# Kernel optimization log

Hardware: AMD Instinct MI355X
Metric: run time of the kernel (lower is better)

## Reference

```python
import jax, jax.numpy as jnp
import numpy as np

B, N, K, C = 2, 4096, 2048, 16
DSPAN, E, H, V = 2048, 300, 512, 100000
WEIGHT = 1.0


def setup_inputs() -> dict:
    key = jax.random.key(0)
    ks = jax.random.split(key, 10)
    return {
        "cand_span_vecs": jax.random.normal(ks[0], (B, N, DSPAN), jnp.float32),
        "targets_all": jax.random.uniform(ks[1], (B, N, C), jnp.float32),
        "entity_emb": jax.random.normal(ks[2], (V, E), jnp.float32) * 0.02,
        "W1": jax.random.normal(ks[3], (DSPAN + E, H), jnp.float32) * 0.02,
        "b1": jnp.zeros((H,), jnp.float32),
        "W2": jax.random.normal(ks[4], (H, 1), jnp.float32) * 0.02,
        "b2": jnp.zeros((1,), jnp.float32),
        "linker_indices_hoi": jax.random.randint(ks[5], (B, K), 0, N, jnp.int64),
        "candidates_all": jax.random.randint(ks[6], (B, N, C), 0, V, jnp.int64),
        "candidate_lengths_all": jax.random.randint(ks[7], (B, N), 0, C + 1, jnp.int64),
    }


def reference(cand_span_vecs, targets_all, entity_emb, W1, b1, W2, b2,
              linker_indices_hoi, candidates_all, candidate_lengths_all):
    idx = linker_indices_hoi  # [B, K]
    # batched_index_select over the span axis
    candidates = jnp.take_along_axis(candidates_all, idx[:, :, None], axis=1)      # [B,K,C]
    cand_lens = jnp.take_along_axis(candidate_lengths_all, idx, axis=1)            # [B,K]
    targets = jnp.take_along_axis(targets_all, idx[:, :, None], axis=1)            # [B,K,C]
    linker_vecs = jnp.take_along_axis(cand_span_vecs, idx[:, :, None], axis=1)     # [B,K,Dspan]
    # entity embedding lookup
    candidate_vecs = entity_emb[candidates]                                        # [B,K,C,E]
    # expand span vecs over candidate axis and concat
    span_exp = jnp.broadcast_to(linker_vecs[:, :, None, :],
                                (linker_vecs.shape[0], linker_vecs.shape[1],
                                 candidate_vecs.shape[2], linker_vecs.shape[2]))
    vecs = jnp.concatenate([span_exp, candidate_vecs], axis=-1)                    # [B,K,C,Dspan+E]
    # FFNN: Linear -> ReLU -> (dropout is identity in eval) -> Linear
    h = jax.nn.relu(jnp.einsum('bkcd,dh->bkch', vecs, W1) + b1)
    scores = (jnp.einsum('bkch,ho->bkco', h, W2) + b2)[..., 0]                     # [B,K,C]
    # candidate mask: valid where position < candidate_length
    mask = (jnp.arange(scores.shape[-1]) < cand_lens[:, :, None]).astype(scores.dtype)
    # BCEWithLogits (reduction='none'): softplus(x) - x*t
    bce = jax.nn.softplus(scores) - scores * targets
    obj = (mask * bce).sum() * WEIGHT
    return obj
```

## Files before the change

kernel.cpp:

```cpp
#include <hip/hip_runtime.h>
#include <math.h>

#define NN 4096
#define CC 16
#define DSP 2048
#define ED 300
#define HD 512

typedef __attribute__((ext_vector_type(8))) short short8;
typedef __attribute__((ext_vector_type(4))) float f32x4;

#define MFMA16(a, b, c) __builtin_amdgcn_mfma_f32_16x16x32_bf16((a), (b), (c), 0, 0, 0)

__device__ __forceinline__ unsigned short f2bf(float x) {
    unsigned u = __builtin_bit_cast(unsigned, x);
    u += 0x7FFFu + ((u >> 16) & 1u);
    return (unsigned short)(u >> 16);
}

__device__ __forceinline__ float bf2f(unsigned short u) {
    return __builtin_bit_cast(float, (unsigned)u << 16);
}

__device__ __forceinline__ void gl_lds16(const void* g, void* l) {
    __builtin_amdgcn_global_load_lds(
        (const __attribute__((address_space(1))) unsigned*)g,
        (__attribute__((address_space(3))) unsigned*)l, 16, 0, 0);
}

__device__ __forceinline__ void pack8(unsigned short* dst, float4 a, float4 b) {
    unsigned short v[8] = { f2bf(a.x), f2bf(a.y), f2bf(a.z), f2bf(a.w),
                            f2bf(b.x), f2bf(b.y), f2bf(b.z), f2bf(b.w) };
    *(short8*)dst = *(short8*)v;
}

__global__ __launch_bounds__(256) void prep_gather_scan(
    const float* __restrict__ W1,
    const float* __restrict__ span,
    const int*   __restrict__ lidx,
    const int*   __restrict__ clens,
    unsigned short* __restrict__ W1sT,
    unsigned short* __restrict__ w1ef,
    unsigned short* __restrict__ A16,
    int*            __restrict__ off)
{
    const int bid = blockIdx.x, tid = threadIdx.x;

    if (bid == 4432) {
        __shared__ int ls[256];
        int myl[16];
        int msum = 0;
#pragma unroll
        for (int j = 0; j < 16; ++j) {
            int bk = tid * 16 + j;
            size_t base = (size_t)(bk >> 11) * NN + lidx[bk];
            int len = clens[base];
            len = len < 0 ? 0 : (len > CC ? CC : len);
            myl[j] = len; msum += len;
        }
        ls[tid] = msum;
        __syncthreads();
        for (int d = 1; d < 256; d <<= 1) {
            int v = (tid >= d) ? ls[tid - d] : 0;
            __syncthreads();
            ls[tid] += v;
            __syncthreads();
        }
        int run = ls[tid] - msum;
#pragma unroll
        for (int j = 0; j < 16; ++j) { off[tid * 16 + j] = run; run += myl[j]; }
        if (tid == 255) off[4096] = run;
        return;
    }
    if (bid >= 336) {
        const int bk = bid - 336;
        const float* src = span + ((size_t)(bk >> 11) * NN + lidx[bk]) * DSP;
        float4 x = *(const float4*)(src + tid * 8);
        float4 y = *(const float4*)(src + tid * 8 + 4);
        pack8(&A16[(size_t)bk * DSP + tid * 8], x, y);
        return;
    }
    if (bid < 256) {
        __shared__ float t[64][65];
        const int k0 = (bid >> 3) * 64, n0 = (bid & 7) * 64;
#pragma unroll
        for (int p = 0; p < 16; ++p) {
            int flat = p * 256 + tid;
            int r = flat >> 6, c = flat & 63;
            t[r][c] = W1[(size_t)(k0 + r) * HD + n0 + c];
        }
        __syncthreads();
#pragma unroll
        for (int p = 0; p < 16; ++p) {
            int flat = p * 256 + tid;
            int c = flat >> 6, r = flat & 63;
            W1sT[(size_t)(n0 + c) * DSP + k0 + r] = f2bf(t[r][c]);
        }
    } else {
        int t0 = (bid - 256) * 256 + tid;
        int lane = t0 & 63;
        int ks = (t0 >> 6) % 10;
        int ncg = (t0 >> 6) / 10;
        int col = ncg * 16 + (lane & 15);
        int kb = ks * 32 + ((lane >> 4) << 3);
        unsigned short v[8];
#pragma unroll
        for (int j = 0; j < 8; ++j) {
            int k = kb + j;
            v[j] = (k < ED) ? f2bf(W1[(size_t)(DSP + k) * HD + col]) : (unsigned short)0;
        }
        *(short8*)&w1ef[(size_t)t0 * 8] = *(short8*)v;
    }
}

__global__ __launch_bounds__(256) void gemm_and_fill(
    const unsigned short* __restrict__ A16,
    const unsigned short* __restrict__ BT,
    const float* __restrict__ b1,
    unsigned short* __restrict__ Cout,
    const int* __restrict__ lidx,
    const int* __restrict__ cands,
    const int* __restrict__ clens,
    const int* __restrict__ off,
    int* __restrict__ compact_cand,
    int* __restrict__ compact_meta)
{
    const int tid = threadIdx.x;

    if (blockIdx.x >= 512) {
        int fb = blockIdx.x - 512;
        int item0 = (fb * 256 + tid) * 4;
#pragma unroll
        for (int q = 0; q < 4; ++q) {
            int item = item0 + q;
            int bk = item >> 4, c = item & 15;
            size_t base = (size_t)(bk >> 11) * NN + lidx[bk];
            int len = clens[base];
            len = len > CC ? CC : len;
            if (c < len) {
                int pos = off[bk] + c;
                compact_cand[pos] = cands[base * CC + c];
                compact_meta[pos] = item;
            }
        }
        return;
    }

    __shared__ __align__(16) unsigned short As[4][64 * 64];
    __shared__ __align__(16) unsigned short Bs[4][64 * 64];
    const int l = tid & 63, wid = tid >> 6;
    const int wr = (wid >> 1) * 32, wc = (wid & 1) * 32;

    const int bid = blockIdx.x;
    const int brow = ((bid & 7) * 8 + ((bid >> 3) >> 3)) * 64;
    const int bcol = (((bid >> 3) & 7)) * 64;

    const int s0 = tid, s1 = tid + 256;
    const int r0 = s0 >> 3, c0 = ((s0 & 7) ^ (r0 & 7)) * 8;
    const int r1 = s1 >> 3, c1 = ((s1 & 7) ^ (r1 & 7)) * 8;
    const unsigned short* ga0 = A16 + (size_t)(brow + r0) * DSP + c0;
    const unsigned short* ga1 = A16 + (size_t)(brow + r1) * DSP + c1;
    const unsigned short* gb0 = BT + (size_t)(bcol + r0) * DSP + c0;
    const unsigned short* gb1 = BT + (size_t)(bcol + r1) * DSP + c1;

    int offA[2][2], offB[2][2];
#pragma unroll
    for (int mf = 0; mf < 2; ++mf) {
        int row = wr + mf * 16 + (l & 15);
#pragma unroll
        for (int kk = 0; kk < 2; ++kk)
            offA[mf][kk] = row * 64 + (((kk * 4) + (l >> 4)) ^ (row & 7)) * 8;
    }
#pragma unroll
    for (int nf = 0; nf < 2; ++nf) {
        int row = wc + nf * 16 + (l & 15);
#pragma unroll
        for (int kk = 0; kk < 2; ++kk)
            offB[nf][kk] = row * 64 + (((kk * 4) + (l >> 4)) ^ (row & 7)) * 8;
    }

    f32x4 z = {0.f, 0.f, 0.f, 0.f};
    f32x4 acc[2][2] = {{z, z}, {z, z}};

    auto stage = [&](int buf, int t) {
        const int k0 = t * 64;
        gl_lds16(ga0 + k0, &As[buf][s0 * 8]);
        gl_lds16(ga1 + k0, &As[buf][s1 * 8]);
        gl_lds16(gb0 + k0, &Bs[buf][s0 * 8]);
        gl_lds16(gb1 + k0, &Bs[buf][s1 * 8]);
    };

    auto compute = [&](int buf) {
        short8 am[2][2], bn[2][2];
#pragma unroll
        for (int mf = 0; mf < 2; ++mf)
#pragma unroll
            for (int kk = 0; kk < 2; ++kk)
                am[mf][kk] = *(const short8*)&As[buf][offA[mf][kk]];
#pragma unroll
        for (int nf = 0; nf < 2; ++nf)
#pragma unroll
            for (int kk = 0; kk < 2; ++kk)
                bn[nf][kk] = *(const short8*)&Bs[buf][offB[nf][kk]];
#pragma unroll
        for (int m = 0; m < 2; ++m)
#pragma unroll
            for (int n = 0; n < 2; ++n)
#pragma unroll
                for (int kk = 0; kk < 2; ++kk)
                    acc[m][n] = MFMA16(am[m][kk], bn[n][kk], acc[m][n]);
    };

    stage(0, 0);
    stage(1, 1);
    stage(2, 2);

    for (int t = 0; t < 29; ++t) {
        asm volatile("s_waitcnt vmcnt(8)" ::: "memory");
        __builtin_amdgcn_s_barrier();
        stage((t + 3) & 3, t + 3);
        compute(t & 3);
    }
    asm volatile("s_waitcnt vmcnt(8)" ::: "memory");
    __builtin_amdgcn_s_barrier();
    compute(29 & 3);
    asm volatile("s_waitcnt vmcnt(4)" ::: "memory");
    __builtin_amdgcn_s_barrier();
    compute(30 & 3);
    asm volatile("s_waitcnt vmcnt(0)" ::: "memory");
    __builtin_amdgcn_s_barrier();
    compute(31 & 3);

#pragma unroll
    for (int n = 0; n < 2; ++n) {
        int col = bcol + wc + n * 16 + (l & 15);
        float b1v = b1[col];
#pragma unroll
        for (int m = 0; m < 2; ++m) {
            int row0 = brow + wr + m * 16 + (l >> 4) * 4;
#pragma unroll
            for (int r = 0; r < 4; ++r)
                Cout[(size_t)(row0 + r) * HD + col] = f2bf(acc[m][n][r] + b1v);
        }
    }
}

__global__ __launch_bounds__(512) void ent_mfma(
    const unsigned short* __restrict__ w1ef,
    const unsigned short* __restrict__ span_part,
    const float* __restrict__ emb,
    const float* __restrict__ W2,
    const float* __restrict__ b2,
    const int*   __restrict__ lidx,
    const float* __restrict__ targets,
    const int*   __restrict__ compact_cand,
    const int*   __restrict__ compact_meta,
    const int*   __restrict__ off,
    float* __restrict__ blockPartial)
{
    const int total = off[4096];
    const int bid = blockIdx.x;
    const int slotBase = bid * 128;
    const int tid = threadIdx.x;
    if (slotBase >= total) {
        if (tid == 0) blockPartial[bid] = 0.f;
        return;
    }

    __shared__ __align__(16) unsigned short As[2][8 * 64 * 8];
    __shared__ float shp[8][16][8];
    __shared__ int   meta_s[128];
    __shared__ float wred[8];
    const int wid = tid >> 6, l = tid & 63;

    if (tid < 128) {
        int slot = slotBase + tid;
        meta_s[tid] = (slot < total) ? compact_meta[slot] : -1;
    }

    const int slot_s = slotBase + wid * 16 + (l & 15);
    const int cid = (slot_s < total) ? compact_cand[slot_s] : 0;
    const float* erow = emb + (size_t)cid * ED;
    const int kb = (l >> 4) * 8;
    const int ht = wid;

    float4 lx = *(const float4*)(erow + kb);
    float4 ly = *(const float4*)(erow + kb + 4);
    pack8(&As[0][tid * 8], lx, ly);
    __syncthreads();

    f32x4 z = {0.f, 0.f, 0.f, 0.f};
    f32x4 acc[8][4];
#pragma unroll
    for (int g = 0; g < 8; ++g)
#pragma unroll
        for (int nc = 0; nc < 4; ++nc) acc[g][nc] = z;

    int cur = 0;
    for (int ks = 0; ks < 10; ++ks) {
        const bool pf = (ks < 9);
        if (pf) {
            int k = (ks + 1) * 32 + kb;
            if (k + 8 <= ED) {
                lx = *(const float4*)(erow + k);
                ly = *(const float4*)(erow + k + 4);
            } else {
                float tmp[8];
#pragma unroll
                for (int j = 0; j < 8; ++j) tmp[j] = (k + j < ED) ? erow[k + j] : 0.f;
                lx = make_float4(tmp[0], tmp[1], tmp[2], tmp[3]);
                ly = make_float4(tmp[4], tmp[5], tmp[6], tmp[7]);
            }
        }
        short8 af[8];
#pragma unroll
        for (int g = 0; g < 8; ++g)
            af[g] = *(const short8*)&As[cur][(g * 64 + l) * 8];
#pragma unroll
        for (int nc = 0; nc < 4; ++nc) {
            short8 bf = *(const short8*)&w1ef[(((size_t)(ht * 4 + nc) * 10 + ks) * 64 + l) * 8];
#pragma unroll
            for (int g = 0; g < 8; ++g)
                acc[g][nc] = MFMA16(af[g], bf, acc[g][nc]);
        }
        if (pf) {
            pack8(&As[cur ^ 1][tid * 8], lx, ly);
        }
        __syncthreads();
        cur ^= 1;
    }

    float w2v[4];
#pragma unroll
    for (int nc = 0; nc < 4; ++nc) w2v[nc] = W2[ht * 64 + nc * 16 + (l & 15)];
    const int rq = (l >> 4) * 4;

#pragma unroll
    for (int g = 0; g < 8; ++g) {
        int bkR[4];
#pragma unroll
        for (int i = 0; i < 4; ++i) {
            int m = meta_s[g * 16 + rq + i];
            bkR[i] = (m >= 0) ? (m >> 4) : 0;
        }
        float s[4] = {0.f, 0.f, 0.f, 0.f};
#pragma unroll
        for (int nc = 0; nc < 4; ++nc) {
            int col = ht * 64 + nc * 16 + (l & 15);
            f32x4 a = acc[g][nc];
#pragma unroll
            for (int i = 0; i < 4; ++i) {
                float sp = bf2f(span_part[(size_t)bkR[i] * HD + col]);
                s[i] += fmaxf(a[i] + sp, 0.f) * w2v[nc];
            }
        }
#pragma unroll
        for (int m = 1; m < 16; m <<= 1) {
#pragma unroll
            for (int i = 0; i < 4; ++i) s[i] += __shfl_xor(s[i], m, 64);
        }
        if ((l & 15) == 0) {
#pragma unroll
            for (int i = 0; i < 4; ++i) shp[g][rq + i][ht] = s[i];
        }
    }
    __syncthreads();

    float val = 0.f;
    if (tid < 128) {
        int m = meta_s[tid];
        if (m >= 0) {
            int bk = m >> 4, c = m & 15;
            size_t base = (size_t)(bk >> 11) * NN + lidx[bk];
            const float* p = &shp[tid >> 4][tid & 15][0];
            float sc = ((p[0] + p[1]) + (p[2] + p[3])) +
                       ((p[4] + p[5]) + (p[6] + p[7])) + b2[0];
            float tg = targets[base * CC + c];
            val = fmaxf(sc, 0.f) + log1pf(expf(-fabsf(sc))) - sc * tg;
        }
    }
#pragma unroll
    for (int m = 32; m; m >>= 1) val += __shfl_xor(val, m, 64);
    if (l == 0) wred[wid] = val;
    __syncthreads();
    if (tid == 0) {
        float s = 0.f;
#pragma unroll
        for (int w = 0; w < 8; ++w) s += wred[w];
        blockPartial[bid] = s;
    }
}

__global__ __launch_bounds__(256) void final_reduce(
    const float* __restrict__ bp, float* __restrict__ out)
{
    __shared__ float red[4];
    float s = bp[threadIdx.x] + bp[threadIdx.x + 256];
#pragma unroll
    for (int m = 32; m; m >>= 1) s += __shfl_xor(s, m, 64);
    if ((threadIdx.x & 63) == 0) red[threadIdx.x >> 6] = s;
    __syncthreads();
    if (threadIdx.x == 0)
        out[0] = (red[0] + red[1]) + (red[2] + red[3]);
}

extern "C" void kernel_launch(void* const* d_in, const int* in_sizes, int n_in,
                              void* d_out, int out_size, void* d_ws, size_t ws_size,
                              hipStream_t stream) {
    const float* span    = (const float*)d_in[0];
    const float* targets = (const float*)d_in[1];
    const float* emb     = (const float*)d_in[2];
    const float* W1      = (const float*)d_in[3];
    const float* b1      = (const float*)d_in[4];
    const float* W2      = (const float*)d_in[5];
    const float* b2      = (const float*)d_in[6];
    const int*   lidx    = (const int*)d_in[7];
    const int*   cands   = (const int*)d_in[8];
    const int*   clens   = (const int*)d_in[9];

    char* ws = (char*)d_ws;
    unsigned short* W1sT      = (unsigned short*)(ws);
    unsigned short* w1ef      = (unsigned short*)(ws + 2097152);
    unsigned short* A16       = (unsigned short*)(ws + 2424832);
    unsigned short* span_part = (unsigned short*)(ws + 19202048);
    int*            off       = (int*)(ws + 23396352);
    int*            ccand     = (int*)(ws + 23412740);
    int*            cmeta     = (int*)(ws + 23674884);
    float*          bpart     = (float*)(ws + 23937028);

    prep_gather_scan<<<4433, 256, 0, stream>>>(W1, span, lidx, clens,
                                               W1sT, w1ef, A16, off);
    gemm_and_fill<<<576, 256, 0, stream>>>(A16, W1sT, b1, span_part,
                                           lidx, cands, clens, off, ccand, cmeta);
    ent_mfma<<<512, 512, 0, stream>>>(w1ef, span_part, emb, W2, b2,
                                      lidx, targets, ccand, cmeta, off, bpart);
    final_reduce<<<1, 256, 0, stream>>>(bpart, (float*)d_out);
}
```

Measured before the change: 62.96 us.

## Fuse final reduction into ent_mfma via ticket counter; halve block tile to 64 slots

Removes the separate final_reduce launch: each ent_mfma block writes its partial, increments an atomic ticket, and the last block to arrive sums all partials and writes the output. The ticket is reset inside prep_gather_scan. ent_mfma also changes from 512-thread blocks covering 128 slots to 256-thread blocks covering 64 slots, launched as 1024 blocks, with each wave now owning 128 hidden columns. The aim is to cut one launch and raise block count for better load balance. In exchange, each block reads its B fragments (w1ef) for half as many rows, and the last-block pattern adds an atomic and a fence per block.

Measured after the change: 97.03 us. 54.1% more time.

```diff
diff --git a/kernel.cpp b/kernel.cpp
--- a/kernel.cpp
+++ b/kernel.cpp
@@ -42,11 +42,13 @@
     unsigned short* __restrict__ W1sT,
     unsigned short* __restrict__ w1ef,
     unsigned short* __restrict__ A16,
-    int*            __restrict__ off)
+    int*            __restrict__ off,
+    unsigned*       __restrict__ ticket)
 {
     const int bid = blockIdx.x, tid = threadIdx.x;
 
     if (bid == 4432) {
+        if (tid == 0) *ticket = 0u;
         __shared__ int ls[256];
         int myl[16];
         int msum = 0;
@@ -245,7 +247,7 @@
     }
 }
 
-__global__ __launch_bounds__(512) void ent_mfma(
+__global__ __launch_bounds__(256) void ent_mfma(
     const unsigned short* __restrict__ w1ef,
     const unsigned short* __restrict__ span_part,
     const float* __restrict__ emb,
@@ -256,152 +258,150 @@
     const int*   __restrict__ compact_cand,
     const int*   __restrict__ compact_meta,
     const int*   __restrict__ off,
-    float* __restrict__ blockPartial)
+    float*       __restrict__ blockPartial,
+    unsigned*    __restrict__ ticket,
+    float*       __restrict__ out)
 {
     const int total = off[4096];
     const int bid = blockIdx.x;
-    const int slotBase = bid * 128;
+    const int slotBase = bid * 64;
     const int tid = threadIdx.x;
-    if (slotBase >= total) {
-        if (tid == 0) blockPartial[bid] = 0.f;
-        return;
-    }
-
-    __shared__ __align__(16) unsigned short As[2][8 * 64 * 8];
-    __shared__ float shp[8][16][8];
-    __shared__ int   meta_s[128];
-    __shared__ float wred[8];
     const int wid = tid >> 6, l = tid & 63;
 
-    if (tid < 128) {
-        int slot = slotBase + tid;
-        meta_s[tid] = (slot < total) ? compact_meta[slot] : -1;
-    }
-
-    const int slot_s = slotBase + wid * 16 + (l & 15);
-    const int cid = (slot_s < total) ? compact_cand[slot_s] : 0;
-    const float* erow = emb + (size_t)cid * ED;
-    const int kb = (l >> 4) * 8;
-    const int ht = wid;
-
-    float4 lx = *(const float4*)(erow + kb);
-    float4 ly = *(const float4*)(erow + kb + 4);
-    pack8(&As[0][tid * 8], lx, ly);
+    __shared__ __align__(16) unsigned short As[2][4 * 64 * 8];
+    __shared__ float shp[4][16][4];
+    __shared__ int   meta_s[64];
+    __shared__ unsigned tk;
+
+    float bsum = 0.f;
+
+    if (slotBase < total) {
+        if (tid < 64) {
+            int slot = slotBase + tid;
+            meta_s[tid] = (slot < total) ? compact_meta[slot] : -1;
+        }
+
+        const int slot_s = slotBase + wid * 16 + (l & 15);
+        const int cid = (slot_s < total) ? compact_cand[slot_s] : 0;
+        const float* erow = emb + (size_t)cid * ED;
+        const int kb = (l >> 4) * 8;
+
+        float4 lx = *(const float4*)(erow + kb);
+        float4 ly = *(const float4*)(erow + kb + 4);
+        pack8(&As[0][tid * 8], lx, ly);
+        __syncthreads();
+
+        f32x4 z = {0.f, 0.f, 0.f, 0.f};
+        f32x4 acc[4][8];
+#pragma unroll
+        for (int g = 0; g < 4; ++g)
+#pragma unroll
+            for (int nc = 0; nc < 8; ++nc) acc[g][nc] = z;
+
+        int cur = 0;
+        for (int ks = 0; ks < 10; ++ks) {
+            const bool pf = (ks < 9);
+            if (pf) {
+                int k = (ks + 1) * 32 + kb;
+                if (k + 8 <= ED) {
+                    lx = *(const float4*)(erow + k);
+                    ly = *(const float4*)(erow + k + 4);
+                } else {
+                    float tmp[8];
+#pragma unroll
+                    for (int j = 0; j < 8; ++j) tmp[j] = (k + j < ED) ? erow[k + j] : 0.f;
+                    lx = make_float4(tmp[0], tmp[1], tmp[2], tmp[3]);
+                    ly = make_float4(tmp[4], tmp[5], tmp[6], tmp[7]);
+                }
+            }
+            short8 af[4];
+#pragma unroll
+            for (int g = 0; g < 4; ++g)
+                af[g] = *(const short8*)&As[cur][(g * 64 + l) * 8];
+#pragma unroll
+            for (int nc = 0; nc < 8; ++nc) {
+                short8 bf = *(const short8*)&w1ef[(((size_t)(wid * 8 + nc) * 10 + ks) * 64 + l) * 8];
+#pragma unroll
+                for (int g = 0; g < 4; ++g)
+                    acc[g][nc] = MFMA16(af[g], bf, acc[g][nc]);
+            }
+            if (pf) {
+                pack8(&As[cur ^ 1][tid * 8], lx, ly);
+            }
+            __syncthreads();
+            cur ^= 1;
+        }
+
+        float w2v[8];
+#pragma unroll
+        for (int nc = 0; nc < 8; ++nc) w2v[nc] = W2[wid * 128 + nc * 16 + (l & 15)];
+        const int rq = (l >> 4) * 4;
+
+#pragma unroll
+        for (int g = 0; g < 4; ++g) {
+            int bkR[4];
+#pragma unroll
+            for (int i = 0; i < 4; ++i) {
+                int m = meta_s[g * 16 + rq + i];
+                bkR[i] = (m >= 0) ? (m >> 4) : 0;
+            }
+            float s[4] = {0.f, 0.f, 0.f, 0.f};
+#pragma unroll
+            for (int nc = 0; nc < 8; ++nc) {
+                int col = wid * 128 + nc * 16 + (l & 15);
+                f32x4 a = acc[g][nc];
+#pragma unroll
+                for (int i = 0; i < 4; ++i) {
+                    float sp = bf2f(span_part[(size_t)bkR[i] * HD + col]);
+                    s[i] += fmaxf(a[i] + sp, 0.f) * w2v[nc];
+                }
+            }
+#pragma unroll
+            for (int m = 1; m < 16; m <<= 1) {
+#pragma unroll
+                for (int i = 0; i < 4; ++i) s[i] += __shfl_xor(s[i], m, 64);
+            }
+            if ((l & 15) == 0) {
+#pragma unroll
+                for (int i = 0; i < 4; ++i) shp[g][rq + i][wid] = s[i];
+            }
+        }
+        __syncthreads();
+
+        if (wid == 0) {
+            float val = 0.f;
+            int m = meta_s[l];
+            if (m >= 0) {
+                int bk = m >> 4, c = m & 15;
+                size_t base = (size_t)(bk >> 11) * NN + lidx[bk];
+                const float* p = &shp[l >> 4][l & 15][0];
+                float sc = (p[0] + p[1]) + (p[2] + p[3]) + b2[0];
+                float tg = targets[base * CC + c];
+                val = fmaxf(sc, 0.f) + log1pf(expf(-fabsf(sc))) - sc * tg;
+            }
+#pragma unroll
+            for (int m2 = 32; m2; m2 >>= 1) val += __shfl_xor(val, m2, 64);
+            bsum = val;
+        }
+    }
+
+    if (tid == 0) {
+        blockPartial[bid] = bsum;
+        __threadfence();
+        tk = atomicAdd(ticket, 1u);
+    }
     __syncthreads();
-
-    f32x4 z = {0.f, 0.f, 0.f, 0.f};
-    f32x4 acc[8][4];
-#pragma unroll
-    for (int g = 0; g < 8; ++g)
-#pragma unroll
-        for (int nc = 0; nc < 4; ++nc) acc[g][nc] = z;
-
-    int cur = 0;
-    for (int ks = 0; ks < 10; ++ks) {
-        const bool pf = (ks < 9);
-        if (pf) {
-            int k = (ks + 1) * 32 + kb;
-            if (k + 8 <= ED) {
-                lx = *(const float4*)(erow + k);
-                ly = *(const float4*)(erow + k + 4);
-            } else {
-                float tmp[8];
-#pragma unroll
-                for (int j = 0; j < 8; ++j) tmp[j] = (k + j < ED) ? erow[k + j] : 0.f;
-                lx = make_float4(tmp[0], tmp[1], tmp[2], tmp[3]);
-                ly = make_float4(tmp[4], tmp[5], tmp[6], tmp[7]);
-            }
-        }
-        short8 af[8];
-#pragma unroll
-        for (int g = 0; g < 8; ++g)
-            af[g] = *(const short8*)&As[cur][(g * 64 + l) * 8];
-#pragma unroll
-        for (int nc = 0; nc < 4; ++nc) {
-            short8 bf = *(const short8*)&w1ef[(((size_t)(ht * 4 + nc) * 10 + ks) * 64 + l) * 8];
-#pragma unroll
-            for (int g = 0; g < 8; ++g)
-                acc[g][nc] = MFMA16(af[g], bf, acc[g][nc]);
-        }
-        if (pf) {
-            pack8(&As[cur ^ 1][tid * 8], lx, ly);
-        }
+    if (tk == gridDim.x - 1) {
+        __threadfence();
+        volatile const float* vb = blockPartial;
+        float s = (vb[tid] + vb[tid + 256]) + (vb[tid + 512] + vb[tid + 768]);
+        __shared__ float red[4];
+#pragma unroll
+        for (int m = 32; m; m >>= 1) s += __shfl_xor(s, m, 64);
+        if ((tid & 63) == 0) red[tid >> 6] = s;
         __syncthreads();
-        cur ^= 1;
-    }
-
-    float w2v[4];
-#pragma unroll
-    for (int nc = 0; nc < 4; ++nc) w2v[nc] = W2[ht * 64 + nc * 16 + (l & 15)];
-    const int rq = (l >> 4) * 4;
-
-#pragma unroll
-    for (int g = 0; g < 8; ++g) {
-        int bkR[4];
-#pragma unroll
-        for (int i = 0; i < 4; ++i) {
-            int m = meta_s[g * 16 + rq + i];
-            bkR[i] = (m >= 0) ? (m >> 4) : 0;
-        }
-        float s[4] = {0.f, 0.f, 0.f, 0.f};
-#pragma unroll
-        for (int nc = 0; nc < 4; ++nc) {
-            int col = ht * 64 + nc * 16 + (l & 15);
-            f32x4 a = acc[g][nc];
-#pragma unroll
-            for (int i = 0; i < 4; ++i) {
-                float sp = bf2f(span_part[(size_t)bkR[i] * HD + col]);
-                s[i] += fmaxf(a[i] + sp, 0.f) * w2v[nc];
-            }
-        }
-#pragma unroll
-        for (int m = 1; m < 16; m <<= 1) {
-#pragma unroll
-            for (int i = 0; i < 4; ++i) s[i] += __shfl_xor(s[i], m, 64);
-        }
-        if ((l & 15) == 0) {
-#pragma unroll
-            for (int i = 0; i < 4; ++i) shp[g][rq + i][ht] = s[i];
-        }
-    }
-    __syncthreads();
-
-    float val = 0.f;
-    if (tid < 128) {
-        int m = meta_s[tid];
-        if (m >= 0) {
-            int bk = m >> 4, c = m & 15;
-            size_t base = (size_t)(bk >> 11) * NN + lidx[bk];
-            const float* p = &shp[tid >> 4][tid & 15][0];
-            float sc = ((p[0] + p[1]) + (p[2] + p[3])) +
-                       ((p[4] + p[5]) + (p[6] + p[7])) + b2[0];
-            float tg = targets[base * CC + c];
-            val = fmaxf(sc, 0.f) + log1pf(expf(-fabsf(sc))) - sc * tg;
-        }
-    }
-#pragma unroll
-    for (int m = 32; m; m >>= 1) val += __shfl_xor(val, m, 64);
-    if (l == 0) wred[wid] = val;
-    __syncthreads();
-    if (tid == 0) {
-        float s = 0.f;
-#pragma unroll
-        for (int w = 0; w < 8; ++w) s += wred[w];
-        blockPartial[bid] = s;
-    }
-}
-
-__global__ __launch_bounds__(256) void final_reduce(
-    const float* __restrict__ bp, float* __restrict__ out)
-{
-    __shared__ float red[4];
-    float s = bp[threadIdx.x] + bp[threadIdx.x + 256];
-#pragma unroll
-    for (int m = 32; m; m >>= 1) s += __shfl_xor(s, m, 64);
-    if ((threadIdx.x & 63) == 0) red[threadIdx.x >> 6] = s;
-    __syncthreads();
-    if (threadIdx.x == 0)
-        out[0] = (red[0] + red[1]) + (red[2] + red[3]);
+        if (tid == 0) out[0] = (red[0] + red[1]) + (red[2] + red[3]);
+    }
 }
 
 extern "C" void kernel_launch(void* const* d_in, const int* in_sizes, int n_in,
@@ -427,12 +427,13 @@
     int*            ccand     = (int*)(ws + 23412740);
     int*            cmeta     = (int*)(ws + 23674884);
     float*          bpart     = (float*)(ws + 23937028);
+    unsigned*       ticket    = (unsigned*)(ws + 23941124);
 
     prep_gather_scan<<<4433, 256, 0, stream>>>(W1, span, lidx, clens,
-                                               W1sT, w1ef, A16, off);
+                                               W1sT, w1ef, A16, off, ticket);
     gemm_and_fill<<<576, 256, 0, stream>>>(A16, W1sT, b1, span_part,
                                            lidx, cands, clens, off, ccand, cmeta);
-    ent_mfma<<<512, 512, 0, stream>>>(w1ef, span_part, emb, W2, b2,
-                                      lidx, targets, ccand, cmeta, off, bpart);
-    final_reduce<<<1, 256, 0, stream>>>(bpart, (float*)d_out);
-}
+    ent_mfma<<<1024, 256, 0, stream>>>(w1ef, span_part, emb, W2, b2,
+                                       lidx, targets, ccand, cmeta, off,
+                                       bpart, ticket, (float*)d_out);
+}
```
